# Performance work log

Measured on AMD Instinct MI355X. Metric: run time of the kernel, lower is better.

## Reference

```python
import jax, jax.numpy as jnp
import numpy as np

KEYS = ["A1", "B2", "E1", "E2", "E3", "E4", "E5"]
DIMS = [1, 1, 2, 2, 2, 2, 2]  # irrep dimensions for D12 point group
H = 8  # num_heads


def setup_inputs() -> dict:
    key = jax.random.key(0)
    ks = jax.random.split(key, 11)
    B, S, M = 8, 1024, 64  # batch, seq_len, multiplicity per key
    inp = {}
    for i, (name, d) in enumerate(zip(KEYS, DIMS)):
        inp[f"x_{name}"] = jax.random.normal(ks[i], (B, S, d, M), dtype=jnp.float32)
    for j, wn in enumerate(["Wq", "Wk", "Wv", "Wo"]):
        # per-key nn.Linear weights [out_mult, in_mult], stacked over the 7 keys
        inp[wn] = jax.random.normal(ks[7 + j], (7, M, M), dtype=jnp.float32) / np.float32(np.sqrt(M))
    return inp


def _split_heads(v):
    # [B,S,d,m] -> [B,H,S,d*mk]
    B, S, d, m = v.shape
    mk = m // H
    return v.reshape(B, S, d, H, mk).transpose(0, 3, 1, 2, 4).reshape(B, H, S, d * mk)


def _combine_heads(v, d):
    # [B,H,S,d*mk] -> [B,S,d,H*mk]
    B, _, S, dmk = v.shape
    mk = dmk // d
    return v.reshape(B, H, S, d, mk).transpose(0, 2, 3, 1, 4).reshape(B, S, d, H * mk)


def _forward(xs, Wq, Wk, Wv, Wo):
    # per-key bias-free linears on the multiplicity (last) axis; nn.Linear does x @ W.T
    qs = [_split_heads(jnp.einsum('bsdi,oi->bsdo', x, Wq[i])) for i, x in enumerate(xs)]
    kks = [_split_heads(jnp.einsum('bsdi,oi->bsdo', x, Wk[i])) for i, x in enumerate(xs)]
    vs = [_split_heads(jnp.einsum('bsdi,oi->bsdo', x, Wv[i])) for i, x in enumerate(xs)]
    Q = jnp.concatenate(qs, axis=-1)  # [B,H,S,D], D = sum d_k*mk = 96
    K = jnp.concatenate(kks, axis=-1)
    scale = np.float32(1.0 / np.sqrt(Q.shape[-1]))
    probs = jax.nn.softmax(jnp.einsum('bhqd,bhkd->bhqk', Q, K) * scale, axis=-1)
    outs = []
    for i, (v, d) in enumerate(zip(vs, DIMS)):
        o = jnp.einsum('bhqk,bhkd->bhqd', probs, v)  # shared softmax over per-key V branches
        o = _combine_heads(o, d)  # [B,S,d,M]
        outs.append(jnp.einsum('bsdi,oi->bsdo', o, Wo[i]))
    # concatenate the 7 per-key outputs along the irrep-dimension axis: [B,S,12,M]
    return jnp.concatenate(outs, axis=2)


def reference(x_A1, x_B2, x_E1, x_E2, x_E3, x_E4, x_E5, Wq, Wk, Wv, Wo):
    xs = [x_A1, x_B2, x_E1, x_E2, x_E3, x_E4, x_E5]
    return _forward(xs, Wq, Wk, Wv, Wo)
```

## Files before the change

### kernel.cpp

```cpp
#include <hip/hip_runtime.h>
#include <stdint.h>

typedef __attribute__((ext_vector_type(8))) short bf16x8;
typedef __attribute__((ext_vector_type(4))) float f32x4;
typedef unsigned short ushort_t;

#define NE 6291456

__device__ __forceinline__ unsigned short f2bf(float f){
  union { float f; unsigned u; } c; c.f = f;
  unsigned u = c.u;
  u = u + 0x7FFFu + ((u >> 16) & 1u);
  return (unsigned short)(u >> 16);
}

__device__ __forceinline__ bf16x8 cvt8(const float* p){
  const float4 a = ((const float4*)p)[0];
  const float4 b = ((const float4*)p)[1];
  bf16x8 r;
  r[0]=(short)f2bf(a.x); r[1]=(short)f2bf(a.y); r[2]=(short)f2bf(a.z); r[3]=(short)f2bf(a.w);
  r[4]=(short)f2bf(b.x); r[5]=(short)f2bf(b.y); r[6]=(short)f2bf(b.z); r[7]=(short)f2bf(b.w);
  return r;
}

__device__ __forceinline__ uint32_t pk2bf(float a, float b){
  uint32_t r;
  asm("v_cvt_pk_bf16_f32 %0, %1, %2" : "=v"(r) : "v"(a), "v"(b));
  return r;
}

__device__ __forceinline__ float exp2x(float x){
  float r;
  asm("v_exp_f32 %0, %1" : "=v"(r) : "v"(x));
  return r;
}

__device__ __forceinline__ void gll16(const ushort_t* g, short* l){
  __builtin_amdgcn_global_load_lds(
      (const __attribute__((address_space(1))) unsigned int*)g,
      (__attribute__((address_space(3))) unsigned int*)l, 16, 0, 0);
}

__device__ __forceinline__ void rr_decode(int rr, int& i, int& dx, int& d){
  if (rr < 2){ i = rr; dx = 0; d = 1; }
  else { i = 2 + ((rr-2)>>1); dx = (rr-2)&1; d = 2; }
}

__global__ __launch_bounds__(256) void wconv(
    const float* __restrict__ Wq, const float* __restrict__ Wk,
    const float* __restrict__ Wv, const float* __restrict__ Wo,
    ushort_t* __restrict__ out)
{
  const int a = blockIdx.y;
  const float* src = (a==0)?Wq:(a==1)?Wk:(a==2)?Wv:Wo;
  const float sc = (a==0) ? 0.14724743479535623f : 1.0f;
  const int i = (blockIdx.x*256 + threadIdx.x)*8;
  float4 v0 = *(const float4*)(src+i);
  float4 v1 = *(const float4*)(src+i+4);
  uint4 o;
  o.x = pk2bf(v0.x*sc, v0.y*sc);
  o.y = pk2bf(v0.z*sc, v0.w*sc);
  o.z = pk2bf(v1.x*sc, v1.y*sc);
  o.w = pk2bf(v1.z*sc, v1.w*sc);
  *(uint4*)(out + (size_t)a*28672 + i) = o;
}

__global__ __launch_bounds__(256) void qkv_proj(
    const float* __restrict__ xA1, const float* __restrict__ xB2,
    const float* __restrict__ xE1, const float* __restrict__ xE2,
    const float* __restrict__ xE3, const float* __restrict__ xE4,
    const float* __restrict__ xE5,
    const ushort_t* __restrict__ Wb4,
    ushort_t* __restrict__ Qg, ushort_t* __restrict__ KVg)
{
  __shared__ short Cl[64*72];

  const int tile = blockIdx.x;
  const int rr = tile >> 7, rt = tile & 127;
  int i, dx, d; rr_decode(rr, i, dx, d);
  const float* xp = (i==0)?xA1:(i==1)?xB2:(i==2)?xE1:(i==3)?xE2:(i==4)?xE3:(i==5)?xE4:xE5;

  const int lane = threadIdx.x & 63;
  const int w    = threadIdx.x >> 6;
  const int lo = lane & 15, hi = lane >> 4;
  const int b8 = (rt >> 4) * 8;
  const int tile64 = rt & 15;

  bf16x8 afr[2];
  {
    const int R = rt*64 + w*16 + lo;
    const float* rp = xp + (size_t)(R*d + dx) * 64;
    afr[0] = cvt8(rp + 8*hi);
    afr[1] = cvt8(rp + 32 + 8*hi);
  }

  {
    const ushort_t* Wb = Wb4 + (size_t)i * 4096;
    #pragma unroll
    for (int ot = 0; ot < 4; ++ot){
      f32x4 acc = {0.f,0.f,0.f,0.f};
      #pragma unroll
      for (int c = 0; c < 2; ++c){
        bf16x8 bfr = *(const bf16x8*)(Wb + (size_t)(lo + 16*ot) * 64 + 32*c + 8*hi);
        acc = __builtin_amdgcn_mfma_f32_16x16x32_bf16(bfr, afr[c], acc, 0, 0, 0);
      }
      uint2 o2;
      o2.x = pk2bf(acc[0], acc[1]);
      o2.y = pk2bf(acc[2], acc[3]);
      int hh = 2*ot + (hi>>1);
      size_t a = (size_t)((b8 + hh)*16 + tile64)*6144
               + (size_t)((w*3 + (rr>>2))*64 + (rr&3)*16 + lo)*8 + 4*(hi&1);
      *(uint2*)(Qg + a) = o2;
    }
  }

  {
    const ushort_t* Wb = Wb4 + (size_t)28672 + (size_t)i * 4096;
    #pragma unroll
    for (int ot = 0; ot < 4; ++ot){
      f32x4 acc = {0.f,0.f,0.f,0.f};
      #pragma unroll
      for (int c = 0; c < 2; ++c){
        bf16x8 bfr = *(const bf16x8*)(Wb + (size_t)(lo + 16*ot) * 64 + 32*c + 8*hi);
        acc = __builtin_amdgcn_mfma_f32_16x16x32_bf16(bfr, afr[c], acc, 0, 0, 0);
      }
      uint2 o2;
      o2.x = pk2bf(acc[0], acc[1]);
      o2.y = pk2bf(acc[2], acc[3]);
      int hh = 2*ot + (hi>>1);
      size_t a = (size_t)((b8 + hh)*32 + tile64*2 + (w>>1))*6144
               + (size_t)(((w&1)*3 + (rr>>2))*64 + (rr&3)*16 + lo)*8 + 4*(hi&1);
      *(uint2*)(KVg + a) = o2;
    }
  }

  {
    const ushort_t* Wb = Wb4 + (size_t)2*28672 + (size_t)i * 4096;
    #pragma unroll
    for (int ot = 0; ot < 4; ++ot){
      f32x4 acc = {0.f,0.f,0.f,0.f};
      #pragma unroll
      for (int c = 0; c < 2; ++c){
        bf16x8 bfr = *(const bf16x8*)(Wb + (size_t)(lo + 16*ot) * 64 + 32*c + 8*hi);
        acc = __builtin_amdgcn_mfma_f32_16x16x32_bf16(afr[c], bfr, acc, 0, 0, 0);
      }
      #pragma unroll
      for (int r = 0; r < 4; ++r)
        Cl[(w*16 + hi*4 + r)*72 + lo + 16*ot] = (short)f2bf(acc[r]);
    }
    __syncthreads();
    #pragma unroll
    for (int cc = 0; cc < 2; ++cc){
      int c2 = threadIdx.x + cc*256;
      int mm = c2 & 7, hh = (c2>>3)&7, sblk = c2>>6;
      int a5 = sblk>>2, slot = sblk&3;
      short tmp[8];
      #pragma unroll
      for (int jj = 0; jj < 8; ++jj){
        int s_j = a5*32 + (jj>>2)*16 + slot*4 + (jj&3);
        tmp[jj] = Cl[s_j*72 + hh*8 + mm];
      }
      int fh = rr>>1, fl = (rr&1)*8 + mm;
      size_t a = (size_t)((b8 + hh)*32 + tile64*2 + a5)*6144 + 3072
               + (size_t)(fh*64 + slot*16 + fl)*8;
      *(bf16x8*)(KVg + a) = *(const bf16x8*)tmp;
    }
  }
}

__global__ __launch_bounds__(256, 4) void attn(
    const ushort_t* __restrict__ Qg,
    const ushort_t* __restrict__ KVg,
    ushort_t* __restrict__ Oc)
{
  __shared__ __align__(16) short KVl[2][6144];

  const int bid = blockIdx.x;
  const int bh = (bid & 7)*8 + ((bid >> 3) & 7);
  const int qt = bid >> 6;
  const int tid = threadIdx.x;
  const int w = tid >> 6, lane = tid & 63;
  const int lo = lane & 15, hi = lane >> 4;
  const size_t qbase  = (size_t)bh * 16 * 6144;
  const size_t kvbase = (size_t)bh * 32 * 6144;

  bf16x8 qf[2][3];
  #pragma unroll
  for (int g = 0; g < 2; ++g){
    int qq = qt*128 + w*32 + g*16;
    const ushort_t* qb = Qg + qbase + (size_t)(qq >> 6)*6144 + (size_t)(((qq>>4)&3)*3)*512;
    #pragma unroll
    for (int c = 0; c < 3; ++c)
      qf[g][c] = *(const bf16x8*)(qb + (c*64 + lane)*8);
  }

  f32x4 acc[6][2];
  #pragma unroll
  for (int ft = 0; ft < 6; ++ft){ acc[ft][0] = (f32x4){0,0,0,0}; acc[ft][1] = (f32x4){0,0,0,0}; }
  float lr[2] = {0.f, 0.f};

#define STAGE(tt, bb) do { \
    const ushort_t* kv_ = KVg + kvbase + (size_t)(tt)*6144 + tid*8; \
    short* l_ = &KVl[bb][tid*8]; \
    gll16(kv_, l_); gll16(kv_ + 2048, l_ + 2048); gll16(kv_ + 4096, l_ + 4096); \
  } while(0)

  STAGE(0, 0);
  __syncthreads();

  for (int t = 0; t < 32; ++t){
    if (t < 31) STAGE(t+1, (t+1)&1);
    const int cb = t & 1;

    f32x4 st[2][2];
    __builtin_amdgcn_s_setprio(1);
    #pragma unroll
    for (int kvb = 0; kvb < 2; ++kvb){
      bf16x8 kf[3];
      #pragma unroll
      for (int c = 0; c < 3; ++c)
        kf[c] = *(const bf16x8*)&KVl[cb][((kvb*3 + c)*64 + lane)*8];
      #pragma unroll
      for (int g = 0; g < 2; ++g){
        f32x4 s = {0.f,0.f,0.f,0.f};
        #pragma unroll
        for (int c = 0; c < 3; ++c)
          s = __builtin_amdgcn_mfma_f32_16x16x32_bf16(kf[c], qf[g][c], s, 0, 0, 0);
        st[g][kvb] = s;
      }
    }
    __builtin_amdgcn_s_setprio(0);

    bf16x8 pb[2];
    #pragma unroll
    for (int g = 0; g < 2; ++g){
      #pragma unroll
      for (int kvb = 0; kvb < 2; ++kvb)
        #pragma unroll
        for (int r = 0; r < 4; ++r){ st[g][kvb][r] = exp2x(st[g][kvb][r]); lr[g] += st[g][kvb][r]; }
      union { uint32_t u[4]; bf16x8 v; } pu;
      pu.u[0] = pk2bf(st[g][0][0], st[g][0][1]);
      pu.u[1] = pk2bf(st[g][0][2], st[g][0][3]);
      pu.u[2] = pk2bf(st[g][1][0], st[g][1][1]);
      pu.u[3] = pk2bf(st[g][1][2], st[g][1][3]);
      pb[g] = pu.v;
    }

    __builtin_amdgcn_s_setprio(1);
    #pragma unroll
    for (int ft = 0; ft < 6; ++ft){
      bf16x8 va = *(const bf16x8*)&KVl[cb][3072 + (ft*64 + lane)*8];
      acc[ft][0] = __builtin_amdgcn_mfma_f32_16x16x32_bf16(va, pb[0], acc[ft][0], 0, 0, 0);
      acc[ft][1] = __builtin_amdgcn_mfma_f32_16x16x32_bf16(va, pb[1], acc[ft][1], 0, 0, 0);
    }
    __builtin_amdgcn_s_setprio(0);

    __syncthreads();
  }
#undef STAGE

  #pragma unroll
  for (int g = 0; g < 2; ++g){
    float l = lr[g];
    l += __shfl_xor(l, 16);
    l += __shfl_xor(l, 32);
    float rl = 1.f / l;
    int q = qt*128 + w*32 + g*16 + lo;
    #pragma unroll
    for (int ft = 0; ft < 6; ++ft){
      uint2 o;
      o.x = pk2bf(acc[ft][g][0]*rl, acc[ft][g][1]*rl);
      o.y = pk2bf(acc[ft][g][2]*rl, acc[ft][g][3]*rl);
      size_t ad = ((size_t)(bh*24 + ft*4 + hi)*1024 + q)*4;
      *(uint2*)(Oc + ad) = o;
    }
  }
}

__global__ __launch_bounds__(256) void out_proj(
    const ushort_t* __restrict__ Oc,
    const ushort_t* __restrict__ Wb4,
    float* __restrict__ out)
{
  const int tile = blockIdx.x;
  const int rr = tile >> 7, rt = tile & 127;
  int i, dx, d; rr_decode(rr, i, dx, d); (void)dx; (void)d;

  const int lane = threadIdx.x & 63;
  const int w    = threadIdx.x >> 6;
  const int lo = lane & 15, hi = lane >> 4;

  bf16x8 afr[2];
  {
    const int R = rt*64 + w*16 + lo;
    const int b = R >> 10, s = R & 1023;
    union { uint2 u2[2]; bf16x8 v; } a0, a1;
    #pragma unroll
    for (int jj = 0; jj < 2; ++jj){
      a0.u2[jj] = *(const uint2*)(Oc + ((size_t)((b*8 + hi)*24 + 2*rr + jj)*1024 + s)*4);
      a1.u2[jj] = *(const uint2*)(Oc + ((size_t)((b*8 + 4 + hi)*24 + 2*rr + jj)*1024 + s)*4);
    }
    afr[0] = a0.v;
    afr[1] = a1.v;
  }

  const ushort_t* Wb = Wb4 + (size_t)3*28672 + (size_t)i * 4096;
  #pragma unroll
  for (int ot = 0; ot < 4; ++ot){
    f32x4 acc = {0.f,0.f,0.f,0.f};
    #pragma unroll
    for (int c = 0; c < 2; ++c){
      bf16x8 bfr = *(const bf16x8*)(Wb + (size_t)(lo + 16*ot) * 64 + 32*c + 8*hi);
      acc = __builtin_amdgcn_mfma_f32_16x16x32_bf16(afr[c], bfr, acc, 0, 0, 0);
    }
    #pragma unroll
    for (int r = 0; r < 4; ++r){
      int bs = rt*64 + w*16 + hi*4 + r;
      out[(size_t)(bs*12 + rr)*64 + lo + 16*ot] = acc[r];
    }
  }
}

extern "C" void kernel_launch(void* const* d_in, const int* in_sizes, int n_in,
                              void* d_out, int out_size, void* d_ws, size_t ws_size,
                              hipStream_t stream)
{
  const float* xA1 = (const float*)d_in[0];
  const float* xB2 = (const float*)d_in[1];
  const float* xE1 = (const float*)d_in[2];
  const float* xE2 = (const float*)d_in[3];
  const float* xE3 = (const float*)d_in[4];
  const float* xE4 = (const float*)d_in[5];
  const float* xE5 = (const float*)d_in[6];
  const float* Wq  = (const float*)d_in[7];
  const float* Wk  = (const float*)d_in[8];
  const float* Wv  = (const float*)d_in[9];
  const float* Wo  = (const float*)d_in[10];

  ushort_t* Qg  = (ushort_t*)d_ws;
  ushort_t* KVg = Qg + NE;
  ushort_t* Oc  = KVg + (size_t)2*NE;
  ushort_t* Wb4 = Oc + NE;

  wconv<<<dim3(14,4), dim3(256), 0, stream>>>(Wq, Wk, Wv, Wo, Wb4);
  qkv_proj<<<dim3(1536), dim3(256), 0, stream>>>(xA1,xB2,xE1,xE2,xE3,xE4,xE5,
                                                 Wb4, Qg, KVg);
  attn<<<dim3(512), dim3(256), 0, stream>>>(Qg, KVg, Oc);
  out_proj<<<dim3(1536), dim3(256), 0, stream>>>(Oc, Wb4, (float*)d_out);
}
```

Before: 71.78 us.

## Split KV sequence across wave pairs in attention with LDS reduction of partials

Each wave now handles 64 queries instead of 32, and the four waves form two query groups times two KV halves. Each KV half streams alternating 64-key tiles through its own double buffer. At the end, the partial accumulators and row sums from the second KV half are combined through LDS before normalization. This halves how often each wave reloads K/V fragments from LDS per query and halves the loop trip count. The cost is higher register pressure (launch bounds drop from 4 to 2 blocks per SIMD), twice the LDS footprint, and an extra reduction step.

```diff
diff --git a/kernel.cpp b/kernel.cpp
--- a/kernel.cpp
+++ b/kernel.cpp
@@ -168,60 +168,66 @@
   }
 }
 
-__global__ __launch_bounds__(256, 4) void attn(
+__global__ __launch_bounds__(256, 2) void attn(
     const ushort_t* __restrict__ Qg,
     const ushort_t* __restrict__ KVg,
     ushort_t* __restrict__ Oc)
 {
-  __shared__ __align__(16) short KVl[2][6144];
+  __shared__ __align__(16) short KVl[2][2][6144];
+  __shared__ float Lx[2][4][64];
 
   const int bid = blockIdx.x;
   const int bh = (bid & 7)*8 + ((bid >> 3) & 7);
   const int qt = bid >> 6;
   const int tid = threadIdx.x;
   const int w = tid >> 6, lane = tid & 63;
+  const int wq = w & 1, wk = w >> 1;
   const int lo = lane & 15, hi = lane >> 4;
   const size_t qbase  = (size_t)bh * 16 * 6144;
   const size_t kvbase = (size_t)bh * 32 * 6144;
 
-  bf16x8 qf[2][3];
+  bf16x8 qf[4][3];
+  {
+    const ushort_t* qb = Qg + qbase + (size_t)(2*qt + wq)*6144;
+    #pragma unroll
+    for (int g = 0; g < 4; ++g)
+      #pragma unroll
+      for (int c = 0; c < 3; ++c)
+        qf[g][c] = *(const bf16x8*)(qb + ((g*3 + c)*64 + lane)*8);
+  }
+
+  f32x4 acc[6][4];
   #pragma unroll
-  for (int g = 0; g < 2; ++g){
-    int qq = qt*128 + w*32 + g*16;
-    const ushort_t* qb = Qg + qbase + (size_t)(qq >> 6)*6144 + (size_t)(((qq>>4)&3)*3)*512;
-    #pragma unroll
-    for (int c = 0; c < 3; ++c)
-      qf[g][c] = *(const bf16x8*)(qb + (c*64 + lane)*8);
-  }
-
-  f32x4 acc[6][2];
-  #pragma unroll
-  for (int ft = 0; ft < 6; ++ft){ acc[ft][0] = (f32x4){0,0,0,0}; acc[ft][1] = (f32x4){0,0,0,0}; }
-  float lr[2] = {0.f, 0.f};
-
-#define STAGE(tt, bb) do { \
-    const ushort_t* kv_ = KVg + kvbase + (size_t)(tt)*6144 + tid*8; \
-    short* l_ = &KVl[bb][tid*8]; \
-    gll16(kv_, l_); gll16(kv_ + 2048, l_ + 2048); gll16(kv_ + 4096, l_ + 4096); \
+  for (int ft = 0; ft < 6; ++ft)
+    #pragma unroll
+    for (int g = 0; g < 4; ++g) acc[ft][g] = (f32x4){0,0,0,0};
+  float lr[4] = {0.f, 0.f, 0.f, 0.f};
+
+#define STAGE(jj, bb) do { \
+    const ushort_t* kv_ = KVg + kvbase + (size_t)(2*(jj)+wk)*6144 + wq*3072 + lane*8; \
+    short* l_ = &KVl[wk][bb][wq*3072 + lane*8]; \
+    gll16(kv_,        l_);        gll16(kv_ + 512,  l_ + 512); \
+    gll16(kv_ + 1024, l_ + 1024); gll16(kv_ + 1536, l_ + 1536); \
+    gll16(kv_ + 2048, l_ + 2048); gll16(kv_ + 2560, l_ + 2560); \
   } while(0)
 
   STAGE(0, 0);
   __syncthreads();
 
-  for (int t = 0; t < 32; ++t){
-    if (t < 31) STAGE(t+1, (t+1)&1);
-    const int cb = t & 1;
-
-    f32x4 st[2][2];
+  for (int j = 0; j < 16; ++j){
+    if (j < 15) STAGE(j+1, (j+1)&1);
+    const short* kb = &KVl[wk][j&1][0];
+
+    f32x4 st[4][2];
     __builtin_amdgcn_s_setprio(1);
     #pragma unroll
     for (int kvb = 0; kvb < 2; ++kvb){
       bf16x8 kf[3];
       #pragma unroll
       for (int c = 0; c < 3; ++c)
-        kf[c] = *(const bf16x8*)&KVl[cb][((kvb*3 + c)*64 + lane)*8];
-      #pragma unroll
-      for (int g = 0; g < 2; ++g){
+        kf[c] = *(const bf16x8*)&kb[((kvb*3 + c)*64 + lane)*8];
+      #pragma unroll
+      for (int g = 0; g < 4; ++g){
         f32x4 s = {0.f,0.f,0.f,0.f};
         #pragma unroll
         for (int c = 0; c < 3; ++c)
@@ -231,9 +237,9 @@
     }
     __builtin_amdgcn_s_setprio(0);
 
-    bf16x8 pb[2];
-    #pragma unroll
-    for (int g = 0; g < 2; ++g){
+    bf16x8 pb[4];
+    #pragma unroll
+    for (int g = 0; g < 4; ++g){
       #pragma unroll
       for (int kvb = 0; kvb < 2; ++kvb)
         #pragma unroll
@@ -249,9 +255,10 @@
     __builtin_amdgcn_s_setprio(1);
     #pragma unroll
     for (int ft = 0; ft < 6; ++ft){
-      bf16x8 va = *(const bf16x8*)&KVl[cb][3072 + (ft*64 + lane)*8];
-      acc[ft][0] = __builtin_amdgcn_mfma_f32_16x16x32_bf16(va, pb[0], acc[ft][0], 0, 0, 0);
-      acc[ft][1] = __builtin_amdgcn_mfma_f32_16x16x32_bf16(va, pb[1], acc[ft][1], 0, 0, 0);
+      bf16x8 va = *(const bf16x8*)&kb[3072 + (ft*64 + lane)*8];
+      #pragma unroll
+      for (int g = 0; g < 4; ++g)
+        acc[ft][g] = __builtin_amdgcn_mfma_f32_16x16x32_bf16(va, pb[g], acc[ft][g], 0, 0, 0);
     }
     __builtin_amdgcn_s_setprio(0);
 
@@ -260,19 +267,38 @@
 #undef STAGE
 
   #pragma unroll
-  for (int g = 0; g < 2; ++g){
-    float l = lr[g];
-    l += __shfl_xor(l, 16);
-    l += __shfl_xor(l, 32);
-    float rl = 1.f / l;
-    int q = qt*128 + w*32 + g*16 + lo;
+  for (int g = 0; g < 4; ++g){
+    lr[g] += __shfl_xor(lr[g], 16);
+    lr[g] += __shfl_xor(lr[g], 32);
+  }
+
+  float* facc = (float*)&KVl[0][0][0];
+  if (wk == 1){
+    #pragma unroll
+    for (int ft = 0; ft < 6; ++ft)
+      #pragma unroll
+      for (int g = 0; g < 4; ++g)
+        *(f32x4*)&facc[(((wq*6 + ft)*4 + g)*64 + lane)*4] = acc[ft][g];
+    #pragma unroll
+    for (int g = 0; g < 4; ++g) Lx[wq][g][lane] = lr[g];
+  }
+  __syncthreads();
+  if (wk == 0){
+    float rl[4];
+    #pragma unroll
+    for (int g = 0; g < 4; ++g) rl[g] = 1.f / (lr[g] + Lx[wq][g][lane]);
     #pragma unroll
     for (int ft = 0; ft < 6; ++ft){
-      uint2 o;
-      o.x = pk2bf(acc[ft][g][0]*rl, acc[ft][g][1]*rl);
-      o.y = pk2bf(acc[ft][g][2]*rl, acc[ft][g][3]*rl);
-      size_t ad = ((size_t)(bh*24 + ft*4 + hi)*1024 + q)*4;
-      *(uint2*)(Oc + ad) = o;
+      #pragma unroll
+      for (int g = 0; g < 4; ++g){
+        f32x4 o = acc[ft][g] + *(const f32x4*)&facc[(((wq*6 + ft)*4 + g)*64 + lane)*4];
+        uint2 ou;
+        ou.x = pk2bf(o[0]*rl[g], o[1]*rl[g]);
+        ou.y = pk2bf(o[2]*rl[g], o[3]*rl[g]);
+        int q = qt*128 + wq*64 + g*16 + lo;
+        size_t ad = ((size_t)(bh*24 + ft*4 + hi)*1024 + q)*4;
+        *(uint2*)(Oc + ad) = ou;
+      }
     }
   }
 }
```

New measurement: 71.69 us (median of 2 runs). Within noise of the previous version (-0.1%).
